# Performance work log

Measured on AMD Instinct MI355X. Metric: run time of the kernel, lower is better.

Reference implementation:

```python
import jax, jax.numpy as jnp
import numpy as np

N, C_IN, C_OUT, W_DIM, H, W = 16, 512, 512, 512, 64, 64

def setup_inputs() -> dict:
    key = jax.random.key(0)
    ks = jax.random.split(key, 6)
    return {
        "x": jax.random.normal(ks[0], (N, C_IN, H, W), dtype=jnp.float32),
        "w": jax.random.normal(ks[1], (N, W_DIM), dtype=jnp.float32),
        "noise": jax.random.normal(ks[2], (N, 1, H, W), dtype=jnp.float32),
        "affine_w": jax.random.normal(ks[3], (C_IN, W_DIM), dtype=jnp.float32) * (1.0 / np.sqrt(W_DIM)),
        "affine_b": jnp.ones((C_IN,), dtype=jnp.float32),  # bias_init=1.0
        "noise_strength": jnp.ones((), dtype=jnp.float32),
        "conv_w": jax.random.normal(ks[4], (C_OUT, C_IN, 3, 3), dtype=jnp.float32),
        "conv_b": jnp.zeros((C_OUT,), dtype=jnp.float32),
    }

def reference(x, w, noise, affine_w, affine_b, noise_strength, conv_w, conv_b):
    # affine: s = w @ affine_w.T + affine_b  (no activation)
    s = jnp.einsum('nd,cd->nc', w, affine_w) + affine_b  # [N, C_in]
    # Demodulated per-sample conv. Original builds w_n = W * s_n then demodulates;
    # since conv is linear in the weight's input-channel scale, this is equivalent to
    # scaling the input by s and the output by the demod factor d.
    w2 = jnp.sum(conv_w * conv_w, axis=(2, 3))  # [O, I]: sum over kernel taps
    d = jax.lax.rsqrt(jnp.einsum('ni,oi->no', s * s, w2) + 1e-8)  # [N, O]
    x_mod = x * s[:, :, None, None]
    y = jax.lax.conv_general_dilated(
        x_mod, conv_w, window_strides=(1, 1), padding='SAME',
        dimension_numbers=('NCHW', 'OIHW', 'NCHW'))  # [N, O, H, W]
    y = y * d[:, :, None, None] + conv_b[None, :, None, None]
    y = y + noise * noise_strength
    return jnp.where(y >= 0, y, 0.2 * y)  # LeakyReLU(0.2)
```

## Files before the change

### kernel.cpp

```cpp
#include <hip/hip_runtime.h>
#include <hip/hip_bf16.h>

typedef unsigned short u16;
typedef short bf16x8 __attribute__((ext_vector_type(8)));
typedef float f32x4 __attribute__((ext_vector_type(4)));

#define N_    16
#define CIN   512
#define COUT  512
#define WD    512
#define P_    4096

#define OFF_S   0u
#define OFF_D   32768u
#define OFF_Z   65536u
#define OFF_WBT 131072u
#define OFF_XB  8388608u
#define WS_NEED (OFF_XB + 67108864u)

__device__ __forceinline__ u16 f2bf(float f) {
  union { float f; unsigned u; } a; a.f = f;
  unsigned r = a.u + 0x7fffu + ((a.u >> 16) & 1u);
  return (u16)(r >> 16);
}

__device__ __forceinline__ void gl_lds16(const u16* g, u16* l) {
  __builtin_amdgcn_global_load_lds(
      (const __attribute__((address_space(1))) void*)g,
      (__attribute__((address_space(3))) void*)l, 16, 0, 0);
}

__global__ void k_zero(float* z) { z[threadIdx.x] = 0.f; }

__global__ __launch_bounds__(256) void k_affine(const float* __restrict__ w,
                                                const float* __restrict__ aw,
                                                const float* __restrict__ ab,
                                                float* __restrict__ s) {
  int idx = blockIdx.x * 256 + threadIdx.x;
  int n = idx >> 9, c = idx & 511;
  const float4* wr = (const float4*)(w + (size_t)n * WD);
  const float4* ar = (const float4*)(aw + (size_t)c * WD);
  float acc = 0.f;
#pragma unroll 4
  for (int k = 0; k < WD / 4; ++k) {
    float4 a = wr[k], b = ar[k];
    acc += a.x * b.x + a.y * b.y + a.z * b.z + a.w * b.w;
  }
  s[idx] = acc + ab[c];
}

__global__ __launch_bounds__(256) void k_demod(const float* __restrict__ s,
                                               const float* __restrict__ cw,
                                               float* __restrict__ d) {
  __shared__ float w2[CIN];
  int o = blockIdx.x;
  const float* wr = cw + (size_t)o * CIN * 9;
  for (int i = threadIdx.x; i < CIN; i += 256) {
    float acc = 0.f;
#pragma unroll
    for (int t = 0; t < 9; ++t) { float v = wr[i * 9 + t]; acc += v * v; }
    w2[i] = acc;
  }
  __syncthreads();
  int wave = threadIdx.x >> 6, lane = threadIdx.x & 63;
  for (int nn = wave; nn < N_; nn += 4) {
    float acc = 0.f;
    for (int i = lane; i < CIN; i += 64) {
      float sv = s[nn * CIN + i];
      acc += sv * sv * w2[i];
    }
#pragma unroll
    for (int off = 32; off > 0; off >>= 1) acc += __shfl_down(acc, off);
    if (lane == 0) {
      float a = acc + 1e-8f;
      float r = rsqrtf(a);
      r = r * (1.5f - 0.5f * a * r * r);
      d[nn * COUT + o] = r;
    }
  }
}

__global__ __launch_bounds__(256) void k_wprep(const float* __restrict__ cw,
                                               u16* __restrict__ wbt) {
  int idx = blockIdx.x * 256 + threadIdx.x;
  if (idx >= COUT * CIN * 9) return;
  int t = idx % 9; int oi = idx / 9; int i = oi & 511; int o = oi >> 9;
  wbt[((size_t)t * COUT + o) * CIN + i] = f2bf(cw[idx]);
}

__global__ __launch_bounds__(256) void k_xmod(const float* __restrict__ x,
                                              const float* __restrict__ s,
                                              u16* __restrict__ xb) {
  __shared__ float tile[64][65];
  int b = blockIdx.x;
  int pt = b & 63; int ct = (b >> 6) & 7; int n = b >> 9;
  int c0 = ct * 64, p0 = pt * 64;
  const float* xp = x + ((size_t)n * CIN + c0) * P_ + p0;
  int t = threadIdx.x;
#pragma unroll
  for (int pass = 0; pass < 4; ++pass) {
    int r = pass * 16 + (t >> 4);
    int col4 = (t & 15);
    float4 v = *(const float4*)(xp + (size_t)r * P_ + col4 * 4);
    float sc = s[n * CIN + c0 + r];
    tile[r][col4 * 4 + 0] = v.x * sc;
    tile[r][col4 * 4 + 1] = v.y * sc;
    tile[r][col4 * 4 + 2] = v.z * sc;
    tile[r][col4 * 4 + 3] = v.w * sc;
  }
  __syncthreads();
  int p = t >> 2, cq = (t & 3) * 16;
  union { u16 us[16]; uint4 q[2]; } pk;
#pragma unroll
  for (int j = 0; j < 16; ++j) pk.us[j] = f2bf(tile[cq + j][p]);
  uint4* dst = (uint4*)(xb + ((size_t)n * P_ + p0 + p) * CIN + c0 + cq);
  dst[0] = pk.q[0];
  dst[1] = pk.q[1];
}

__global__ __launch_bounds__(512, 1) void k_conv(const u16* __restrict__ xb,
                                                 const u16* __restrict__ wbt,
                                                 const u16* __restrict__ zp,
                                                 const float* __restrict__ dmod,
                                                 const float* __restrict__ cbias,
                                                 const float* __restrict__ noise,
                                                 const float* __restrict__ nstr,
                                                 float* __restrict__ out) {
  __shared__ u16 smA[4][8192];
  __shared__ u16 smB[4][8192];

  int bid = blockIdx.x;
  int wg = (bid & 7) * 64 + (bid >> 3);
  int n = wg >> 5;
  int rem = wg & 31;
  int ob = rem >> 4;
  int pb = rem & 15;

  int tid = threadIdx.x;
  int wv = tid >> 6, l = tid & 63;
  int wr = wv >> 2, wc = wv & 3;
  int lrow = l & 15, kgrp = l >> 4;
  int prs = kgrp ^ ((lrow >> 1) & 3);

  int srow = tid >> 2;
  int lslot = (tid & 3) ^ ((tid >> 3) & 3);
  const u16* xbn = xb + (size_t)n * P_ * CIN;
  int hg[2], wgp[2];
#pragma unroll
  for (int g = 0; g < 2; ++g) {
    int ploc = g * 128 + srow;
    hg[g] = pb * 4 + (ploc >> 6);
    wgp[g] = ploc & 63;
  }
  const u16* srcA_base[2];
#pragma unroll
  for (int g = 0; g < 2; ++g)
    srcA_base[g] = wbt + (size_t)(ob * 256 + g * 128 + srow) * CIN + lslot * 8;

  auto stage_A = [&](int tt) {
    int b = tt & 3;
    int tapn = tt >> 4, cbn = tt & 15;
#pragma unroll
    for (int g = 0; g < 2; ++g) {
      const u16* src = srcA_base[g] + (size_t)tapn * (COUT * CIN) + cbn * 32;
      gl_lds16(src, &smA[b][g * 4096 + wv * 512]);
    }
  };
  auto stage_B = [&](int tt) {
    int b = tt & 3;
    int tapn = tt >> 4, cbn = tt & 15;
    int q = (tapn * 11) >> 5;
    int dh = q - 1, dw = tapn - q * 3 - 1;
#pragma unroll
    for (int g = 0; g < 2; ++g) {
      int hh = hg[g] + dh, ww = wgp[g] + dw;
      bool val = ((unsigned)hh < 64u) && ((unsigned)ww < 64u);
      const u16* src = val ? (xbn + ((size_t)((hh << 6) + ww)) * CIN + cbn * 32 + lslot * 8)
                           : (zp + lslot * 8);
      gl_lds16(src, &smB[b][g * 4096 + wv * 512]);
    }
  };

  f32x4 acc0[4][4], acc1[4][4];
  f32x4 zero = {0.f, 0.f, 0.f, 0.f};
#pragma unroll
  for (int i = 0; i < 4; ++i)
#pragma unroll
    for (int j = 0; j < 4; ++j) { acc0[i][j] = zero; acc1[i][j] = zero; }

  stage_A(0); stage_B(0);
  stage_A(1); stage_B(1);

  for (int t = 0; t < 144; ++t) {
    int b = t & 3;
    if (t < 143) asm volatile("s_waitcnt vmcnt(4)" ::: "memory");
    else         asm volatile("s_waitcnt vmcnt(0)" ::: "memory");
    __builtin_amdgcn_s_barrier();
    __builtin_amdgcn_sched_barrier(0);

    const u16* A = smA[b];
    const u16* B = smB[b];
    bf16x8 Af[4], Bf[4];
#pragma unroll
    for (int ni = 0; ni < 4; ++ni)
      Bf[ni] = *(const bf16x8*)&B[(wc * 64 + ni * 16 + lrow) * 32 + prs * 8];
#pragma unroll
    for (int mi = 0; mi < 4; ++mi)
      Af[mi] = *(const bf16x8*)&A[(wr * 128 + mi * 16 + lrow) * 32 + prs * 8];
    if (t < 142) stage_A(t + 2);
    __builtin_amdgcn_s_setprio(1);
#pragma unroll
    for (int mi = 0; mi < 4; ++mi)
#pragma unroll
      for (int ni = 0; ni < 4; ++ni)
        acc0[mi][ni] = __builtin_amdgcn_mfma_f32_16x16x32_bf16(
            Af[mi], Bf[ni], acc0[mi][ni], 0, 0, 0);
    __builtin_amdgcn_s_setprio(0);

#pragma unroll
    for (int mi = 0; mi < 4; ++mi)
      Af[mi] = *(const bf16x8*)&A[(wr * 128 + 64 + mi * 16 + lrow) * 32 + prs * 8];
    if (t < 142) stage_B(t + 2);
    __builtin_amdgcn_s_setprio(1);
#pragma unroll
    for (int mi = 0; mi < 4; ++mi)
#pragma unroll
      for (int ni = 0; ni < 4; ++ni)
        acc1[mi][ni] = __builtin_amdgcn_mfma_f32_16x16x32_bf16(
            Af[mi], Bf[ni], acc1[mi][ni], 0, 0, 0);
    __builtin_amdgcn_s_setprio(0);
  }

  float ns = nstr[0];
  const float* noise_n = noise + (size_t)n * P_;
  float nz[4];
#pragma unroll
  for (int ni = 0; ni < 4; ++ni)
    nz[ni] = noise_n[pb * 256 + wc * 64 + ni * 16 + lrow] * ns;

  auto epi = [&](f32x4 (&A_)[4][4], int qm) {
#pragma unroll
    for (int mi = 0; mi < 4; ++mi) {
      int o0 = ob * 256 + wr * 128 + qm * 64 + mi * 16 + kgrp * 4;
#pragma unroll
      for (int r = 0; r < 4; ++r) {
        int o = o0 + r;
        float dv = dmod[n * COUT + o];
        float bv = cbias[o];
        float* orow = out + ((size_t)(n * COUT + o)) * P_ + pb * 256 + wc * 64;
#pragma unroll
        for (int ni = 0; ni < 4; ++ni) {
          float v = A_[mi][ni][r] * dv + bv + nz[ni];
          orow[ni * 16 + lrow] = v >= 0.f ? v : 0.2f * v;
        }
      }
    }
  };
  epi(acc0, 0);
  epi(acc1, 1);
}

__global__ __launch_bounds__(64) void k_conv_naive(const float* __restrict__ x,
                                                   const float* __restrict__ cw,
                                                   const float* __restrict__ cbias,
                                                   const float* __restrict__ noise,
                                                   const float* __restrict__ nstr,
                                                   const float* __restrict__ s,
                                                   const float* __restrict__ d,
                                                   float* __restrict__ out) {
  int bid = blockIdx.x;
  int h = bid & 63; int o = (bid >> 6) & 511; int n = bid >> 15;
  int wcol = threadIdx.x;
  float acc = 0.f;
  for (int i = 0; i < CIN; ++i) {
    float sv = s[n * CIN + i];
    const float* xrow = x + ((size_t)(n * CIN + i)) * P_;
    const float* wrp = cw + ((size_t)o * CIN + i) * 9;
#pragma unroll
    for (int t = 0; t < 9; ++t) {
      int hh = h + t / 3 - 1, ww = wcol + t % 3 - 1;
      float xv = ((unsigned)hh < 64u && (unsigned)ww < 64u) ? xrow[hh * 64 + ww] : 0.f;
      acc += xv * sv * wrp[t];
    }
  }
  float v = acc * d[n * COUT + o] + cbias[o] + noise[(size_t)n * P_ + h * 64 + wcol] * nstr[0];
  out[((size_t)(n * COUT + o)) * P_ + h * 64 + wcol] = v >= 0.f ? v : 0.2f * v;
}

extern "C" void kernel_launch(void* const* d_in, const int* in_sizes, int n_in,
                              void* d_out, int out_size, void* d_ws, size_t ws_size,
                              hipStream_t stream) {
  const float* x    = (const float*)d_in[0];
  const float* w    = (const float*)d_in[1];
  const float* noise= (const float*)d_in[2];
  const float* aw   = (const float*)d_in[3];
  const float* ab   = (const float*)d_in[4];
  const float* nstr = (const float*)d_in[5];
  const float* cw   = (const float*)d_in[6];
  const float* cb   = (const float*)d_in[7];
  float* out = (float*)d_out;
  char* ws = (char*)d_ws;
  float* s = (float*)(ws + OFF_S);
  float* d = (float*)(ws + OFF_D);

  k_affine<<<(N_ * COUT) / 256, 256, 0, stream>>>(w, aw, ab, s);
  k_demod<<<COUT, 256, 0, stream>>>(s, cw, d);

  if (ws_size >= WS_NEED) {
    u16* zp  = (u16*)(ws + OFF_Z);
    u16* wbt = (u16*)(ws + OFF_WBT);
    u16* xbb = (u16*)(ws + OFF_XB);
    k_zero<<<1, 256, 0, stream>>>((float*)zp);
    k_wprep<<<(COUT * CIN * 9 + 255) / 256, 256, 0, stream>>>(cw, wbt);
    k_xmod<<<N_ * 8 * 64, 256, 0, stream>>>(x, s, xbb);
    k_conv<<<512, 512, 0, stream>>>(xbb, wbt, zp, d, cb, noise, nstr, out);
  } else {
    k_conv_naive<<<N_ * COUT * 64, 64, 0, stream>>>(x, cw, cb, noise, nstr, s, d, out);
  }
}
```

Before: 346.3 us.

## Deepen global-to-LDS prefetch to three stages with incremental source pointers

Raises the prefetch distance in the implicit-GEMM conv main loop from two to three tiles in flight over the 4-slot LDS ring, adjusting the vmcnt waits to match. Per-tile address computation is replaced by running pointers that advance by 32 channels and are recomputed only at tap boundaries. It also adds explicit lgkmcnt waits and an extra mid-iteration barrier. The barrier and waits add synchronisation that could offset the gain from hiding more load latency.

```diff
diff --git a/kernel.cpp b/kernel.cpp
--- a/kernel.cpp
+++ b/kernel.cpp
@@ -10,6 +10,7 @@
 #define COUT  512
 #define WD    512
 #define P_    4096
+#define CC    (COUT * CIN)
 
 #define OFF_S   0u
 #define OFF_D   32768u
@@ -162,23 +163,24 @@
     int tapn = tt >> 4, cbn = tt & 15;
 #pragma unroll
     for (int g = 0; g < 2; ++g) {
-      const u16* src = srcA_base[g] + (size_t)tapn * (COUT * CIN) + cbn * 32;
+      const u16* src = srcA_base[g] + (size_t)tapn * CC + cbn * 32;
       gl_lds16(src, &smA[b][g * 4096 + wv * 512]);
     }
+  };
+  auto bsrc_for_tap = [&](int tapn, int g) -> const u16* {
+    int dh = tapn < 3 ? -1 : (tapn < 6 ? 0 : 1);
+    int dw = tapn - (dh + 1) * 3 - 1;
+    int hh = hg[g] + dh, ww = wgp[g] + dw;
+    bool val = ((unsigned)hh < 64u) && ((unsigned)ww < 64u);
+    return val ? (xbn + ((size_t)((hh << 6) + ww)) * CIN + lslot * 8)
+               : (zp + lslot * 8);
   };
   auto stage_B = [&](int tt) {
     int b = tt & 3;
     int tapn = tt >> 4, cbn = tt & 15;
-    int q = (tapn * 11) >> 5;
-    int dh = q - 1, dw = tapn - q * 3 - 1;
-#pragma unroll
-    for (int g = 0; g < 2; ++g) {
-      int hh = hg[g] + dh, ww = wgp[g] + dw;
-      bool val = ((unsigned)hh < 64u) && ((unsigned)ww < 64u);
-      const u16* src = val ? (xbn + ((size_t)((hh << 6) + ww)) * CIN + cbn * 32 + lslot * 8)
-                           : (zp + lslot * 8);
-      gl_lds16(src, &smB[b][g * 4096 + wv * 512]);
-    }
+#pragma unroll
+    for (int g = 0; g < 2; ++g)
+      gl_lds16(bsrc_for_tap(tapn, g) + cbn * 32, &smB[b][g * 4096 + wv * 512]);
   };
 
   f32x4 acc0[4][4], acc1[4][4];
@@ -190,16 +192,29 @@
 
   stage_A(0); stage_B(0);
   stage_A(1); stage_B(1);
+  stage_A(2); stage_B(2);
+
+  int tap3 = 0, cb3 = 3;
+  const u16* rpA[2];
+  const u16* rpB[2];
+#pragma unroll
+  for (int g = 0; g < 2; ++g) {
+    rpA[g] = srcA_base[g] + 3 * 32;
+    rpB[g] = bsrc_for_tap(0, g) + 3 * 32;
+  }
 
   for (int t = 0; t < 144; ++t) {
     int b = t & 3;
-    if (t < 143) asm volatile("s_waitcnt vmcnt(4)" ::: "memory");
-    else         asm volatile("s_waitcnt vmcnt(0)" ::: "memory");
+    int bs = (t + 3) & 3;
+    if (t <= 141)      asm volatile("s_waitcnt vmcnt(8)" ::: "memory");
+    else if (t == 142) asm volatile("s_waitcnt vmcnt(4)" ::: "memory");
+    else               asm volatile("s_waitcnt vmcnt(0)" ::: "memory");
     __builtin_amdgcn_s_barrier();
     __builtin_amdgcn_sched_barrier(0);
 
     const u16* A = smA[b];
     const u16* B = smB[b];
+
     bf16x8 Af[4], Bf[4];
 #pragma unroll
     for (int ni = 0; ni < 4; ++ni)
@@ -207,7 +222,13 @@
 #pragma unroll
     for (int mi = 0; mi < 4; ++mi)
       Af[mi] = *(const bf16x8*)&A[(wr * 128 + mi * 16 + lrow) * 32 + prs * 8];
-    if (t < 142) stage_A(t + 2);
+    if (t <= 140) {
+#pragma unroll
+      for (int g = 0; g < 2; ++g)
+        gl_lds16(rpA[g], &smA[bs][g * 4096 + wv * 512]);
+    }
+    asm volatile("s_waitcnt lgkmcnt(0)" ::: "memory");
+    __builtin_amdgcn_sched_barrier(0);
     __builtin_amdgcn_s_setprio(1);
 #pragma unroll
     for (int mi = 0; mi < 4; ++mi)
@@ -216,11 +237,30 @@
         acc0[mi][ni] = __builtin_amdgcn_mfma_f32_16x16x32_bf16(
             Af[mi], Bf[ni], acc0[mi][ni], 0, 0, 0);
     __builtin_amdgcn_s_setprio(0);
+    __builtin_amdgcn_s_barrier();
 
 #pragma unroll
     for (int mi = 0; mi < 4; ++mi)
       Af[mi] = *(const bf16x8*)&A[(wr * 128 + 64 + mi * 16 + lrow) * 32 + prs * 8];
-    if (t < 142) stage_B(t + 2);
+    if (t <= 140) {
+#pragma unroll
+      for (int g = 0; g < 2; ++g)
+        gl_lds16(rpB[g], &smB[bs][g * 4096 + wv * 512]);
+      cb3++;
+      if (cb3 == 16) {
+        cb3 = 0; tap3++;
+#pragma unroll
+        for (int g = 0; g < 2; ++g) {
+          rpA[g] = srcA_base[g] + (size_t)tap3 * CC;
+          rpB[g] = bsrc_for_tap(tap3, g);
+        }
+      } else {
+#pragma unroll
+        for (int g = 0; g < 2; ++g) { rpA[g] += 32; rpB[g] += 32; }
+      }
+    }
+    asm volatile("s_waitcnt lgkmcnt(0)" ::: "memory");
+    __builtin_amdgcn_sched_barrier(0);
     __builtin_amdgcn_s_setprio(1);
 #pragma unroll
     for (int mi = 0; mi < 4; ++mi)
```

Measured after the change: 342.9 us. No clear change (-1.0%).
